# Kernel optimization log

Hardware: AMD Instinct MI355X
Metric: run time of the kernel (lower is better)

## Reference

```python
import jax, jax.numpy as jnp
import numpy as np
import math

N_A = 100000
N_B = 100000
E = 400000
D = 128      # in_dim == out_dim (skip connection requires equality)
H = 8        # n_heads
DK = 16      # d_k = D // H
SQRT_DK = math.sqrt(DK)


def setup_inputs():
    ks = list(jax.random.split(jax.random.key(0), 32))
    it = iter(ks)

    def nrm(shape, s):
        return (jax.random.normal(next(it), shape) * s).astype(jnp.float32)

    def idx(n):
        return jax.random.randint(next(it), (E,), 0, n)

    inp = {}
    inp['x_a'] = nrm((N_A, D), 1.0)
    inp['x_b'] = nrm((N_B, D), 1.0)
    inp['src_ab'], inp['dst_ab'] = idx(N_A), idx(N_B)
    inp['src_ba'], inp['dst_ba'] = idx(N_B), idx(N_A)
    inp['src_bb'], inp['dst_bb'] = idx(N_B), idx(N_B)
    w_scale = math.sqrt(2.0 / (D + D))  # xavier-ish
    for t in ('a', 'b'):
        for m in ('k', 'q', 'v', 'a'):
            inp['W%s_%s' % (m, t)] = nrm((D, D), w_scale)
            inp['b%s_%s' % (m, t)] = jnp.zeros((D,), jnp.float32)
        inp['skip_%s' % t] = jnp.ones((1,), jnp.float32)
    r_scale = math.sqrt(2.0 / (DK + DK))
    for e in ('ab', 'ba', 'bb'):
        inp['pri_%s' % e] = jnp.ones((H,), jnp.float32)
        inp['att_%s' % e] = nrm((H, DK, DK), r_scale)
        inp['msg_%s' % e] = nrm((H, DK, DK), r_scale)
    return inp


def _etype_agg(k_src, q_dst, v_src, src, dst, att_w, msg_w, pri, n_dst):
    # gather src/dst node features onto edges: [E, H, DK]
    ke = k_src[src]
    # bmm(k.transpose(1,0), relation_att).transpose(1,0) == einsum ehd,hdf->ehf
    key_e = jnp.einsum('ehd,hdf->ehf', ke, att_w)
    a = jnp.sum(q_dst[dst] * key_e, axis=-1) * pri / SQRT_DK   # [E, H]
    val = jnp.einsum('ehd,hdf->ehf', v_src[src], msg_w)         # [E, H, DK]
    # ragged per-dst-node softmax over incoming edges (DGL mailbox softmax)
    amax = jax.ops.segment_max(a, dst, num_segments=n_dst)
    amax = jax.lax.stop_gradient(jnp.where(jnp.isfinite(amax), amax, 0.0))
    ea = jnp.exp(a - amax[dst])
    denom = jax.ops.segment_sum(ea, dst, num_segments=n_dst)
    w = ea / jnp.maximum(denom[dst], 1e-9)
    h = jax.ops.segment_sum(w[:, :, None] * val, dst, num_segments=n_dst)
    return jax.nn.relu(h.reshape(n_dst, H * DK))


def reference(x_a, x_b, src_ab, dst_ab, src_ba, dst_ba, src_bb, dst_bb,
              Wk_a, bk_a, Wq_a, bq_a, Wv_a, bv_a, Wa_a, ba_a, skip_a,
              Wk_b, bk_b, Wq_b, bq_b, Wv_b, bv_b, Wa_b, ba_b, skip_b,
              pri_ab, att_ab, msg_ab, pri_ba, att_ba, msg_ba,
              pri_bb, att_bb, msg_bb):
    n_a, n_b = x_a.shape[0], x_b.shape[0]
    k_a = (x_a @ Wk_a + bk_a).reshape(n_a, H, DK)
    q_a = (x_a @ Wq_a + bq_a).reshape(n_a, H, DK)
    v_a = (x_a @ Wv_a + bv_a).reshape(n_a, H, DK)
    k_b = (x_b @ Wk_b + bk_b).reshape(n_b, H, DK)
    q_b = (x_b @ Wq_b + bq_b).reshape(n_b, H, DK)
    v_b = (x_b @ Wv_b + bv_b).reshape(n_b, H, DK)

    # per-etype attention + softmax + weighted aggregate
    t_b1 = _etype_agg(k_a, q_b, v_a, src_ab, dst_ab, att_ab, msg_ab, pri_ab, n_b)
    t_b2 = _etype_agg(k_b, q_b, v_b, src_bb, dst_bb, att_bb, msg_bb, pri_bb, n_b)
    t_b = 0.5 * (t_b1 + t_b2)        # cross_reducer='mean' over {ab, bb}
    t_a = _etype_agg(k_b, q_a, v_b, src_ba, dst_ba, att_ba, msg_ba, pri_ba, n_a)

    alpha_a = jax.nn.sigmoid(skip_a)
    out_a = (t_a @ Wa_a + ba_a) * alpha_a + x_a * (1.0 - alpha_a)
    alpha_b = jax.nn.sigmoid(skip_b)
    out_b = (t_b @ Wa_b + ba_b) * alpha_b + x_b * (1.0 - alpha_b)
    # dropout is identity in eval; use_norm=False
    return jnp.stack([out_a, out_b])  # [2, N, D]
```

## Files before the change

### kernel.cpp

```cpp
#include <hip/hip_runtime.h>
#include <hip/hip_bf16.h>
#include <stdint.h>

#define D 128
#define H 8
#define DK 16

#define SCAN_BLK 256
#define SCAN_ITEMS 8
#define SCAN_TILE (SCAN_BLK * SCAN_ITEMS)
#define NBUCK 192

typedef __attribute__((ext_vector_type(8))) short bf16x8;
typedef __attribute__((ext_vector_type(4))) float f32x4;

__device__ __forceinline__ unsigned short f2bf(float f) {
    unsigned int u = __float_as_uint(f);
    u = u + 0x7fffu + ((u >> 16) & 1u);
    return (unsigned short)(u >> 16);
}
__device__ __forceinline__ float bfl(unsigned int u) { return __uint_as_float(u << 16); }
__device__ __forceinline__ float bfh(unsigned int u) { return __uint_as_float(u & 0xffff0000u); }
__device__ __forceinline__ unsigned int pack2(unsigned short a, unsigned short b) {
    return (unsigned int)a | ((unsigned int)b << 16);
}
__device__ __forceinline__ void unpack8(uint4 u, float* o) {
    o[0]=bfl(u.x); o[1]=bfh(u.x); o[2]=bfl(u.y); o[3]=bfh(u.y);
    o[4]=bfl(u.z); o[5]=bfh(u.z); o[6]=bfl(u.w); o[7]=bfh(u.w);
}

struct WTIn  { const float* w[4]; };
struct WTOut { unsigned short* wt[4]; };
struct FoldArgs {
    const float* W[6]; const float* R[6]; const float* b[6];
    unsigned short* WT[6]; float* bf[6]; int mode[6];
};

__global__ __launch_bounds__(256) void prep_kernel(WTIn in, WTOut out, FoldArgs a,
                                                   int* __restrict__ cnt, int S,
                                                   int nz, int* __restrict__ dhd) {
    __shared__ float tile[32][33];
    __shared__ float Wl[128 * 17];
    __shared__ float Rl[256];
    int bid = blockIdx.x;
    int tid = threadIdx.x;
    if (bid < 64) {
        int mat = bid >> 4;
        int t = bid & 15;
        int k0 = (t >> 2) * 32, c0 = (t & 3) * 32;
        const float* W = in.w[mat];
        unsigned short* WT = out.wt[mat];
        int lr = tid >> 5, lc = tid & 31;
        #pragma unroll
        for (int p = 0; p < 4; ++p)
            tile[p * 8 + lr][lc] = W[(size_t)(k0 + p * 8 + lr) * D + c0 + lc];
        __syncthreads();
        #pragma unroll
        for (int p = 0; p < 4; ++p)
            WT[(size_t)(c0 + p * 8 + lr) * D + k0 + lc] = f2bf(tile[lc][p * 8 + lr]);
    } else if (bid < 112) {
        int v = (bid - 64) >> 3, h = (bid - 64) & 7;
        const float* W = a.W[v];
        #pragma unroll
        for (int p = 0; p < 8; ++p) {
            int idx = p * 256 + tid;
            int c = idx >> 4, i = idx & 15;
            Wl[c * 17 + i] = W[(size_t)c * D + h * 16 + i];
        }
        Rl[tid] = a.R[v][h * 256 + tid];
        __syncthreads();
        int mode = a.mode[v];
        int c = tid & 127, jb = (tid >> 7) * 8;
        #pragma unroll
        for (int jj = 0; jj < 8; ++jj) {
            int j = jb + jj;
            float s = 0.f;
            #pragma unroll
            for (int i = 0; i < 16; ++i)
                s = fmaf(Wl[c * 17 + i], mode ? Rl[i * 16 + j] : Rl[j * 16 + i], s);
            a.WT[v][(size_t)(h * 16 + j) * D + c] = f2bf(s);
        }
        if (tid < 16) {
            const float* b = a.b[v];
            float s = 0.f;
            #pragma unroll
            for (int i = 0; i < 16; ++i)
                s = fmaf(b[h * 16 + i], mode ? Rl[i * 16 + tid] : Rl[tid * 16 + i], s);
            a.bf[v][h * 16 + tid] = s;
        }
    } else if (bid < 112 + nz) {
        int base = (bid - 112) * 1024 + tid * 4;
        if (base + 4 <= S) {
            *(int4*)&cnt[base] = make_int4(0, 0, 0, 0);
        } else {
            for (int i = base; i < S; ++i) cnt[i] = 0;
        }
    } else {
        for (int i = tid; i < 2 * NBUCK; i += 256) dhd[i] = 0;
    }
}

#define ASTRIDE 136
struct ProjFusedArgs {
    const float* X[2];
    int N[2], nmat[2], nblk0;
    const unsigned short* wt[2][5];
    const float* bias[2][5];
    unsigned short* out[2][5];
};

__global__ __launch_bounds__(256) void proj_fused_kernel(ProjFusedArgs a)
{
    __shared__ unsigned short As[64 * ASTRIDE];
    __shared__ unsigned short Cs[64 * ASTRIDE];
    const int tid = threadIdx.x;
    const int w = tid >> 6;
    const int l = tid & 63;
    const int seg = (blockIdx.x >= a.nblk0) ? 1 : 0;
    const int row0 = (blockIdx.x - (seg ? a.nblk0 : 0)) * 64;
    const float* X = a.X[seg];
    const int N = a.N[seg];
    const int nm = a.nmat[seg];

    #pragma unroll
    for (int p = 0; p < 8; ++p) {
        int f = p * 256 + tid;
        int r = f >> 5;
        int c4 = f & 31;
        int row = row0 + r; if (row >= N) row = N - 1;
        float4 xv = *(const float4*)&X[(size_t)row * D + c4 * 4];
        unsigned int lo = pack2(f2bf(xv.x), f2bf(xv.y));
        unsigned int hi = pack2(f2bf(xv.z), f2bf(xv.w));
        *(uint2*)&As[r * ASTRIDE + c4 * 4] = make_uint2(lo, hi);
    }
    __syncthreads();

    const int lrow = l & 15;
    const int lk8 = (l >> 4) * 8;

    for (int m = 0; m < nm; ++m) {
        const unsigned short* WT = a.wt[seg][m];
        bf16x8 bfrag[2][4];
        #pragma unroll
        for (int cf = 0; cf < 2; ++cf)
            #pragma unroll
            for (int kc = 0; kc < 4; ++kc)
                bfrag[cf][kc] = *(const bf16x8*)&WT[(size_t)(w * 32 + cf * 16 + lrow) * D + kc * 32 + lk8];

        f32x4 acc[4][2];
        #pragma unroll
        for (int rf = 0; rf < 4; ++rf) {
            acc[rf][0] = (f32x4){0.f, 0.f, 0.f, 0.f};
            acc[rf][1] = (f32x4){0.f, 0.f, 0.f, 0.f};
        }
        #pragma unroll
        for (int rf = 0; rf < 4; ++rf) {
            bf16x8 afrag[4];
            #pragma unroll
            for (int kc = 0; kc < 4; ++kc)
                afrag[kc] = *(const bf16x8*)&As[(rf * 16 + lrow) * ASTRIDE + kc * 32 + lk8];
            #pragma unroll
            for (int kc = 0; kc < 4; ++kc) {
                acc[rf][0] = __builtin_amdgcn_mfma_f32_16x16x32_bf16(afrag[kc], bfrag[0][kc], acc[rf][0], 0, 0, 0);
                acc[rf][1] = __builtin_amdgcn_mfma_f32_16x16x32_bf16(afrag[kc], bfrag[1][kc], acc[rf][1], 0, 0, 0);
            }
        }
        float bias0 = a.bias[seg][m][w * 32 + lrow];
        float bias1 = a.bias[seg][m][w * 32 + 16 + lrow];
        #pragma unroll
        for (int rf = 0; rf < 4; ++rf) {
            #pragma unroll
            for (int r = 0; r < 4; ++r) {
                int lr = rf * 16 + (l >> 4) * 4 + r;
                Cs[lr * ASTRIDE + w * 32 + lrow]      = f2bf(acc[rf][0][r] + bias0);
                Cs[lr * ASTRIDE + w * 32 + 16 + lrow] = f2bf(acc[rf][1][r] + bias1);
            }
        }
        __syncthreads();
        unsigned short* O = a.out[seg][m];
        #pragma unroll
        for (int p = 0; p < 4; ++p) {
            int idx = p * 256 + tid;
            int r = idx >> 4, c8 = idx & 15;
            int row = row0 + r;
            if (row < N)
                *(uint4*)&O[(size_t)row * D + c8 * 8] = *(const uint4*)&Cs[r * ASTRIDE + c8 * 8];
        }
        __syncthreads();
    }
}

struct OutFusedArgs {
    const unsigned short* T1[2]; const unsigned short* T2[2];
    const unsigned short* WT[2]; const float* bias[2];
    const float* skip[2]; const float* X[2]; float* O[2];
    int N[2], nsrc[2], nblk0;
};

__global__ __launch_bounds__(256) void out_fused_kernel(OutFusedArgs a)
{
    __shared__ unsigned short As[64 * ASTRIDE];
    const int tid = threadIdx.x;
    const int w = tid >> 6;
    const int l = tid & 63;
    const int seg = (blockIdx.x >= a.nblk0) ? 1 : 0;
    const int row0 = (blockIdx.x - (seg ? a.nblk0 : 0)) * 64;
    const int N = a.N[seg];
    const int nsrc = a.nsrc[seg];
    const unsigned short* T1 = a.T1[seg];
    const unsigned short* T2 = a.T2[seg];

    #pragma unroll
    for (int p = 0; p < 4; ++p) {
        int idx = p * 256 + tid;
        int r = idx >> 4;
        int c8 = idx & 15;
        int row = row0 + r; if (row >= N) row = N - 1;
        uint4 tv = *(const uint4*)&T1[(size_t)row * D + c8 * 8];
        float v[8]; unpack8(tv, v);
        #pragma unroll
        for (int i = 0; i < 8; ++i) v[i] = fmaxf(v[i], 0.f);
        if (nsrc == 2) {
            uint4 uv = *(const uint4*)&T2[(size_t)row * D + c8 * 8];
            float u[8]; unpack8(uv, u);
            #pragma unroll
            for (int i = 0; i < 8; ++i) v[i] = 0.5f * (v[i] + fmaxf(u[i], 0.f));
        }
        uint4 pk;
        pk.x = pack2(f2bf(v[0]), f2bf(v[1]));
        pk.y = pack2(f2bf(v[2]), f2bf(v[3]));
        pk.z = pack2(f2bf(v[4]), f2bf(v[5]));
        pk.w = pack2(f2bf(v[6]), f2bf(v[7]));
        *(uint4*)&As[r * ASTRIDE + c8 * 8] = pk;
    }
    __syncthreads();

    const int lrow = l & 15;
    const int lk8 = (l >> 4) * 8;
    const unsigned short* WT = a.WT[seg];

    bf16x8 bfrag[2][4];
    #pragma unroll
    for (int cf = 0; cf < 2; ++cf)
        #pragma unroll
        for (int kc = 0; kc < 4; ++kc)
            bfrag[cf][kc] = *(const bf16x8*)&WT[(size_t)(w * 32 + cf * 16 + lrow) * D + kc * 32 + lk8];

    f32x4 acc[4][2];
    #pragma unroll
    for (int rf = 0; rf < 4; ++rf) {
        acc[rf][0] = (f32x4){0.f, 0.f, 0.f, 0.f};
        acc[rf][1] = (f32x4){0.f, 0.f, 0.f, 0.f};
    }
    #pragma unroll
    for (int rf = 0; rf < 4; ++rf) {
        bf16x8 afrag[4];
        #pragma unroll
        for (int kc = 0; kc < 4; ++kc)
            afrag[kc] = *(const bf16x8*)&As[(rf * 16 + lrow) * ASTRIDE + kc * 32 + lk8];
        #pragma unroll
        for (int kc = 0; kc < 4; ++kc) {
            acc[rf][0] = __builtin_amdgcn_mfma_f32_16x16x32_bf16(afrag[kc], bfrag[0][kc], acc[rf][0], 0, 0, 0);
            acc[rf][1] = __builtin_amdgcn_mfma_f32_16x16x32_bf16(afrag[kc], bfrag[1][kc], acc[rf][1], 0, 0, 0);
        }
    }
    float alpha = 1.f / (1.f + __expf(-a.skip[seg][0]));
    float om = 1.f - alpha;
    float bias0 = a.bias[seg][w * 32 + lrow];
    float bias1 = a.bias[seg][w * 32 + 16 + lrow];
    const float* X = a.X[seg];
    float* O = a.O[seg];
    #pragma unroll
    for (int rf = 0; rf < 4; ++rf) {
        #pragma unroll
        for (int r = 0; r < 4; ++r) {
            int row = row0 + rf * 16 + (l >> 4) * 4 + r;
            if (row < N) {
                int c0 = w * 32 + lrow;
                float x0 = X[(size_t)row * D + c0];
                float x1 = X[(size_t)row * D + c0 + 16];
                O[(size_t)row * D + c0]      = (acc[rf][0][r] + bias0) * alpha + x0 * om;
                O[(size_t)row * D + c0 + 16] = (acc[rf][1][r] + bias1) * alpha + x1 * om;
            }
        }
    }
}

struct EdgeArgs {
    const int* src[3]; const int* dst[3]; int base[3]; int E;
};

__global__ __launch_bounds__(256) void hist_all_kernel(EdgeArgs a, int* __restrict__ cnt) {
    int gid = blockIdx.x * 256 + threadIdx.x;
    int E = a.E;
    if (gid >= 3 * E) return;
    int t = (gid < E) ? 0 : ((gid < 2 * E) ? 1 : 2);
    int e = gid - t * E;
    atomicAdd(&cnt[a.base[t] + a.dst[t][e]], 1);
}

__global__ __launch_bounds__(SCAN_BLK) void scan1_kernel(
    const int* __restrict__ cnt, int* __restrict__ bsum,
    int* __restrict__ dhist, int n, int n_b)
{
    __shared__ int sh[SCAN_BLK];
    __shared__ int lh[NBUCK];
    int tid = threadIdx.x;
    if (tid < NBUCK) lh[tid] = 0;
    __syncthreads();
    int base = blockIdx.x * SCAN_TILE + tid * SCAN_ITEMS;
    int s = 0;
    #pragma unroll
    for (int i = 0; i < SCAN_ITEMS; ++i) {
        int idx = base + i;
        if (idx < n) {
            int d = cnt[idx];
            s += d;
            int t = (idx < n_b) ? 0 : ((idx < 2 * n_b) ? 1 : 2);
            int dc = d > 63 ? 63 : d;
            atomicAdd(&lh[t * 64 + 63 - dc], 1);
        }
    }
    sh[tid] = s; __syncthreads();
    for (int o = SCAN_BLK / 2; o > 0; o >>= 1) {
        if (tid < o) sh[tid] += sh[tid + o];
        __syncthreads();
    }
    if (tid == 0) bsum[blockIdx.x] = sh[0];
    if (tid < NBUCK && lh[tid]) atomicAdd(&dhist[tid], lh[tid]);
}

__global__ __launch_bounds__(SCAN_BLK) void scan3_kernel(
    const int* __restrict__ cnt, const int* __restrict__ bsum,
    int* __restrict__ offs, int* __restrict__ cursor, int n)
{
    __shared__ int red[SCAN_BLK];
    __shared__ int sh[SCAN_BLK];
    const int tid = threadIdx.x;
    int pre = 0;
    for (int i = tid; i < blockIdx.x; i += SCAN_BLK) pre += bsum[i];
    red[tid] = pre; __syncthreads();
    for (int o = SCAN_BLK / 2; o > 0; o >>= 1) {
        if (tid < o) red[tid] += red[tid + o];
        __syncthreads();
    }
    int base0 = red[0];

    int base = blockIdx.x * SCAN_TILE + tid * SCAN_ITEMS;
    int v[SCAN_ITEMS];
    int s = 0;
    #pragma unroll
    for (int i = 0; i < SCAN_ITEMS; ++i) {
        int idx = base + i;
        v[i] = (idx < n) ? cnt[idx] : 0;
        s += v[i];
    }
    sh[tid] = s; __syncthreads();
    for (int o = 1; o < SCAN_BLK; o <<= 1) {
        int t = (tid >= o) ? sh[tid - o] : 0;
        __syncthreads();
        sh[tid] += t;
        __syncthreads();
    }
    int off = base0 + sh[tid] - s;
    #pragma unroll
    for (int i = 0; i < SCAN_ITEMS; ++i) {
        int idx = base + i;
        if (idx < n) {
            offs[idx] = off;
            cursor[idx] = off;
            off += v[i];
            if (idx == n - 1) offs[n] = off;
        }
    }
}

__global__ __launch_bounds__(256) void scatter_all_kernel(
    EdgeArgs a, int* __restrict__ cursor, int* __restrict__ csr_src)
{
    int gid = blockIdx.x * 256 + threadIdx.x;
    int E = a.E;
    if (gid >= 3 * E) return;
    int t = (gid < E) ? 0 : ((gid < 2 * E) ? 1 : 2);
    int e = gid - t * E;
    int p = atomicAdd(&cursor[a.base[t] + a.dst[t][e]], 1);
    csr_src[p] = a.src[t][e];
}

__global__ __launch_bounds__(256) void deg_scatter_kernel(
    const int* __restrict__ cnt, const int* __restrict__ dhist, int* __restrict__ dcur,
    int* __restrict__ perm, int S, int n_b)
{
    __shared__ int sc[256];
    __shared__ int excl[NBUCK];
    __shared__ int lcnt[NBUCK];
    __shared__ int lbase[NBUCK];
    int tid = threadIdx.x;
    int v = (tid < NBUCK) ? dhist[tid] : 0;
    sc[tid] = v; __syncthreads();
    for (int o = 1; o < 256; o <<= 1) {
        int t = (tid >= o) ? sc[tid - o] : 0;
        __syncthreads();
        sc[tid] += t;
        __syncthreads();
    }
    if (tid < NBUCK) { excl[tid] = sc[tid] - v; lcnt[tid] = 0; }
    __syncthreads();
    int i = blockIdx.x * 256 + tid;
    bool valid = (i < S);
    int b = 0, r = 0;
    if (valid) {
        int t = (i < n_b) ? 0 : ((i < 2 * n_b) ? 1 : 2);
        int d = cnt[i]; if (d > 63) d = 63;
        b = t * 64 + 63 - d;
        r = atomicAdd(&lcnt[b], 1);
    }
    __syncthreads();
    if (tid < NBUCK && lcnt[tid]) lbase[tid] = excl[tid] + atomicAdd(&dcur[tid], lcnt[tid]);
    __syncthreads();
    if (valid) perm[lbase[b] + r] = i;
}

struct AggArgs {
    const unsigned short* K[3];
    const unsigned short* Q[3];
    const unsigned short* V[3];
    const float* pri[3];
    unsigned short* T[3];
};

__global__ __launch_bounds__(256) void csr_agg_all_kernel(
    const int* __restrict__ offs, const int* __restrict__ csr_src,
    const int* __restrict__ perm, AggArgs a, int n_b, int n_a)
{
    int gid = blockIdx.x * 256 + threadIdx.x;
    int si = gid >> 4;
    int hp = gid & 15;
    int h = hp >> 1, p = hp & 1;
    int S = 2 * n_b + n_a;
    if (si >= S) return;
    int s = perm[si];
    int t = (s < n_b) ? 0 : ((s < 2 * n_b) ? 1 : 2);
    int n = s - ((t == 2) ? 2 * n_b : t * n_b);

    const unsigned short *Kp, *Qp, *Vp; const float* prip; unsigned short* Tp;
    if (t == 0)      { Kp=a.K[0]; Qp=a.Q[0]; Vp=a.V[0]; prip=a.pri[0]; Tp=a.T[0]; }
    else if (t == 1) { Kp=a.K[1]; Qp=a.Q[1]; Vp=a.V[1]; prip=a.pri[1]; Tp=a.T[1]; }
    else             { Kp=a.K[2]; Qp=a.Q[2]; Vp=a.V[2]; prip=a.pri[2]; Tp=a.T[2]; }

    int e0 = offs[s], e1 = offs[s + 1];
    const int sub = h * DK + p * 8;

    uint4 q = *(const uint4*)(Qp + (size_t)n * D + sub);
    float qv[8]; unpack8(q, qv);
    float ps = prip[h] * 0.25f;

    float acc[8];
    #pragma unroll
    for (int i = 0; i < 8; ++i) acc[i] = 0.f;
    float den = 0.f;

    for (int e = e0; e < e1; ++e) {
        int sc = csr_src[e];
        uint4 k = *(const uint4*)(Kp + (size_t)sc * D + sub);
        uint4 v = *(const uint4*)(Vp + (size_t)sc * D + sub);
        float kv[8]; unpack8(k, kv);
        float d = 0.f;
        #pragma unroll
        for (int i = 0; i < 8; ++i) d = fmaf(kv[i], qv[i], d);
        d += __shfl_xor(d, 1, 64);
        float ea = __expf(d * ps);
        den += ea;
        float vv[8]; unpack8(v, vv);
        #pragma unroll
        for (int i = 0; i < 8; ++i) acc[i] = fmaf(ea, vv[i], acc[i]);
    }
    float inv = 1.f / fmaxf(den, 1e-9f);
    unsigned short ob[8];
    #pragma unroll
    for (int i = 0; i < 8; ++i) ob[i] = f2bf(acc[i] * inv);
    uint4 o0;
    o0.x = pack2(ob[0], ob[1]);  o0.y = pack2(ob[2], ob[3]);
    o0.z = pack2(ob[4], ob[5]);  o0.w = pack2(ob[6], ob[7]);
    *(uint4*)(Tp + (size_t)n * D + sub) = o0;
}

extern "C" void kernel_launch(void* const* d_in, const int* in_sizes, int n_in,
                              void* d_out, int out_size, void* d_ws, size_t ws_size,
                              hipStream_t stream) {
    const float* x_a = (const float*)d_in[0];
    const float* x_b = (const float*)d_in[1];
    const int* src_ab = (const int*)d_in[2];
    const int* dst_ab = (const int*)d_in[3];
    const int* src_ba = (const int*)d_in[4];
    const int* dst_ba = (const int*)d_in[5];
    const int* src_bb = (const int*)d_in[6];
    const int* dst_bb = (const int*)d_in[7];
    const float* Wk_a = (const float*)d_in[8];  const float* bk_a = (const float*)d_in[9];
    const float* Wq_a = (const float*)d_in[10]; const float* bq_a = (const float*)d_in[11];
    const float* Wv_a = (const float*)d_in[12]; const float* bv_a = (const float*)d_in[13];
    const float* Wa_a = (const float*)d_in[14]; const float* ba_a = (const float*)d_in[15];
    const float* skip_a = (const float*)d_in[16];
    const float* Wk_b = (const float*)d_in[17]; const float* bk_b = (const float*)d_in[18];
    const float* Wq_b = (const float*)d_in[19]; const float* bq_b = (const float*)d_in[20];
    const float* Wv_b = (const float*)d_in[21]; const float* bv_b = (const float*)d_in[22];
    const float* Wa_b = (const float*)d_in[23]; const float* ba_b = (const float*)d_in[24];
    const float* skip_b = (const float*)d_in[25];
    const float* pri_ab = (const float*)d_in[26];
    const float* att_ab = (const float*)d_in[27];
    const float* msg_ab = (const float*)d_in[28];
    const float* pri_ba = (const float*)d_in[29];
    const float* att_ba = (const float*)d_in[30];
    const float* msg_ba = (const float*)d_in[31];
    const float* pri_bb = (const float*)d_in[32];
    const float* att_bb = (const float*)d_in[33];
    const float* msg_bb = (const float*)d_in[34];

    const int n_a = in_sizes[0] / D;
    const int n_b = in_sizes[1] / D;
    const int E = in_sizes[2];
    const int S = 2 * n_b + n_a;

    size_t off = 0;
    char* base = (char*)d_ws;
    auto alloc = [&](size_t bytes) -> void* {
        void* r = base + off;
        off += (bytes + 255) & ~(size_t)255;
        return r;
    };
    unsigned short* k_a = (unsigned short*)alloc((size_t)n_a * D * 2);
    unsigned short* k_b = (unsigned short*)alloc((size_t)n_b * D * 2);
    unsigned short* qab = (unsigned short*)alloc((size_t)n_b * D * 2);
    unsigned short* qbb = (unsigned short*)alloc((size_t)n_b * D * 2);
    unsigned short* qba = (unsigned short*)alloc((size_t)n_a * D * 2);
    unsigned short* vab = (unsigned short*)alloc((size_t)n_a * D * 2);
    unsigned short* vbb = (unsigned short*)alloc((size_t)n_b * D * 2);
    unsigned short* vba = (unsigned short*)alloc((size_t)n_b * D * 2);
    unsigned short* t_a  = (unsigned short*)alloc((size_t)n_a * D * 2);
    unsigned short* t_b1 = (unsigned short*)alloc((size_t)n_b * D * 2);
    unsigned short* t_b2 = (unsigned short*)alloc((size_t)n_b * D * 2);
    int* cnt    = (int*)alloc((size_t)S * 4);
    int* offs   = (int*)alloc(((size_t)S + 1) * 4);
    int* cursor = (int*)alloc((size_t)S * 4);
    int* csr_src= (int*)alloc((size_t)3 * E * 4);
    int* bsum   = (int*)alloc(256 * 4);
    int* dhd    = (int*)alloc(2 * NBUCK * 4);
    int* dhist  = dhd;
    int* dcur   = dhd + NBUCK;
    int* perm   = (int*)alloc((size_t)S * 4);
    unsigned short* wt_plain[4];
    for (int i = 0; i < 4; ++i) wt_plain[i] = (unsigned short*)alloc((size_t)D * D * 2);
    unsigned short* wt_fold[6];
    float* bf_fold[6];
    for (int i = 0; i < 6; ++i) {
        wt_fold[i] = (unsigned short*)alloc((size_t)D * D * 2);
        bf_fold[i] = (float*)alloc((size_t)D * 4);
    }

    WTIn win; WTOut wout;
    const float* worig[4] = {Wk_a, Wk_b, Wa_a, Wa_b};
    for (int i = 0; i < 4; ++i) { win.w[i] = worig[i]; wout.wt[i] = wt_plain[i]; }
    FoldArgs fa;
    const float* fW[6] = {Wq_b, Wq_b, Wq_a, Wv_a, Wv_b, Wv_b};
    const float* fR[6] = {att_ab, att_bb, att_ba, msg_ab, msg_bb, msg_ba};
    const float* fb[6] = {bq_b, bq_b, bq_a, bv_a, bv_b, bv_b};
    int fm[6] = {0, 0, 0, 1, 1, 1};
    for (int i = 0; i < 6; ++i) {
        fa.W[i] = fW[i]; fa.R[i] = fR[i]; fa.b[i] = fb[i];
        fa.WT[i] = wt_fold[i]; fa.bf[i] = bf_fold[i]; fa.mode[i] = fm[i];
    }
    int nz = (S + 1023) / 1024;
    prep_kernel<<<112 + nz + 1, 256, 0, stream>>>(win, wout, fa, cnt, S, nz, dhd);

    EdgeArgs ea;
    ea.src[0] = src_ab; ea.dst[0] = dst_ab;
    ea.src[1] = src_bb; ea.dst[1] = dst_bb;
    ea.src[2] = src_ba; ea.dst[2] = dst_ba;
    ea.base[0] = 0; ea.base[1] = n_b; ea.base[2] = 2 * n_b;
    ea.E = E;
    int ge3 = (3 * E + 255) / 256;
    hist_all_kernel<<<ge3, 256, 0, stream>>>(ea, cnt);
    int nb = (S + SCAN_TILE - 1) / SCAN_TILE;
    scan1_kernel<<<nb, SCAN_BLK, 0, stream>>>(cnt, bsum, dhist, S, n_b);
    scan3_kernel<<<nb, SCAN_BLK, 0, stream>>>(cnt, bsum, offs, cursor, S);
    scatter_all_kernel<<<ge3, 256, 0, stream>>>(ea, cursor, csr_src);

    int gS = (S + 255) / 256;
    deg_scatter_kernel<<<gS, 256, 0, stream>>>(cnt, dhist, dcur, perm, S, n_b);

    const int gb_a = (n_a + 63) / 64;
    const int gb_b = (n_b + 63) / 64;
    ProjFusedArgs pa;
    pa.X[0] = x_a; pa.N[0] = n_a; pa.nmat[0] = 3;
    pa.X[1] = x_b; pa.N[1] = n_b; pa.nmat[1] = 5;
    pa.nblk0 = gb_a;
    pa.wt[0][0] = wt_plain[0]; pa.bias[0][0] = bk_a;       pa.out[0][0] = k_a;
    pa.wt[0][1] = wt_fold[2];  pa.bias[0][1] = bf_fold[2]; pa.out[0][1] = qba;
    pa.wt[0][2] = wt_fold[3];  pa.bias[0][2] = bf_fold[3]; pa.out[0][2] = vab;
    pa.wt[0][3] = wt_plain[0]; pa.bias[0][3] = bk_a;       pa.out[0][3] = k_a;
    pa.wt[0][4] = wt_plain[0]; pa.bias[0][4] = bk_a;       pa.out[0][4] = k_a;
    pa.wt[1][0] = wt_plain[1]; pa.bias[1][0] = bk_b;       pa.out[1][0] = k_b;
    pa.wt[1][1] = wt_fold[0];  pa.bias[1][1] = bf_fold[0]; pa.out[1][1] = qab;
    pa.wt[1][2] = wt_fold[1];  pa.bias[1][2] = bf_fold[1]; pa.out[1][2] = qbb;
    pa.wt[1][3] = wt_fold[4];  pa.bias[1][3] = bf_fold[4]; pa.out[1][3] = vbb;
    pa.wt[1][4] = wt_fold[5];  pa.bias[1][4] = bf_fold[5]; pa.out[1][4] = vba;
    proj_fused_kernel<<<gb_a + gb_b, 256, 0, stream>>>(pa);

    AggArgs aa;
    aa.K[0] = k_a; aa.Q[0] = qab; aa.V[0] = vab; aa.pri[0] = pri_ab; aa.T[0] = t_b1;
    aa.K[1] = k_b; aa.Q[1] = qbb; aa.V[1] = vbb; aa.pri[1] = pri_bb; aa.T[1] = t_b2;
    aa.K[2] = k_b; aa.Q[2] = qba; aa.V[2] = vba; aa.pri[2] = pri_ba; aa.T[2] = t_a;
    int gs = (S * 16 + 255) / 256;
    csr_agg_all_kernel<<<gs, 256, 0, stream>>>(offs, csr_src, perm, aa, n_b, n_a);

    float* out_a = (float*)d_out;
    float* out_b = (float*)d_out + (size_t)n_a * D;
    OutFusedArgs oa;
    oa.T1[0] = t_a;  oa.T2[0] = t_a;  oa.WT[0] = wt_plain[2]; oa.bias[0] = ba_a;
    oa.skip[0] = skip_a; oa.X[0] = x_a; oa.O[0] = out_a; oa.N[0] = n_a; oa.nsrc[0] = 1;
    oa.T1[1] = t_b1; oa.T2[1] = t_b2; oa.WT[1] = wt_plain[3]; oa.bias[1] = ba_b;
    oa.skip[1] = skip_b; oa.X[1] = x_b; oa.O[1] = out_b; oa.N[1] = n_b; oa.nsrc[1] = 2;
    oa.nblk0 = gb_a;
    out_fused_kernel<<<gb_a + gb_b, 256, 0, stream>>>(oa);
}
```

Baseline: 425.1 us.

## Overlap node projection GEMM with CSR build stages and unroll edge loop

Splits the projection GEMM into four chunks and co-schedules each chunk inside the histogram, scan1, scan3 and scatter/degree-sort launches, so independent work fills the otherwise underutilized small CSR-build kernels. This also removes the separate projection launch. Separately, the per-node aggregation loop is unrolled by two edges so the K and V gathers of two neighbors are in flight together. The merged kernels raise shared-memory footprint and register pressure for the light CSR blocks, which may reduce their occupancy.

```diff
diff --git a/kernel.cpp b/kernel.cpp
--- a/kernel.cpp
+++ b/kernel.cpp
@@ -101,23 +101,20 @@
 }
 
 #define ASTRIDE 136
-struct ProjFusedArgs {
+struct ProjChunk {
     const float* X[2];
-    int N[2], nmat[2], nblk0;
+    int N[2], nmat[2];
     const unsigned short* wt[2][5];
     const float* bias[2][5];
     unsigned short* out[2][5];
 };
 
-__global__ __launch_bounds__(256) void proj_fused_kernel(ProjFusedArgs a)
-{
+__device__ __forceinline__ void proj_body(const ProjChunk& a, int seg, int row0) {
     __shared__ unsigned short As[64 * ASTRIDE];
     __shared__ unsigned short Cs[64 * ASTRIDE];
     const int tid = threadIdx.x;
     const int w = tid >> 6;
     const int l = tid & 63;
-    const int seg = (blockIdx.x >= a.nblk0) ? 1 : 0;
-    const int row0 = (blockIdx.x - (seg ? a.nblk0 : 0)) * 64;
     const float* X = a.X[seg];
     const int N = a.N[seg];
     const int nm = a.nmat[seg];
@@ -190,108 +187,18 @@
     }
 }
 
-struct OutFusedArgs {
-    const unsigned short* T1[2]; const unsigned short* T2[2];
-    const unsigned short* WT[2]; const float* bias[2];
-    const float* skip[2]; const float* X[2]; float* O[2];
-    int N[2], nsrc[2], nblk0;
-};
-
-__global__ __launch_bounds__(256) void out_fused_kernel(OutFusedArgs a)
-{
-    __shared__ unsigned short As[64 * ASTRIDE];
-    const int tid = threadIdx.x;
-    const int w = tid >> 6;
-    const int l = tid & 63;
-    const int seg = (blockIdx.x >= a.nblk0) ? 1 : 0;
-    const int row0 = (blockIdx.x - (seg ? a.nblk0 : 0)) * 64;
-    const int N = a.N[seg];
-    const int nsrc = a.nsrc[seg];
-    const unsigned short* T1 = a.T1[seg];
-    const unsigned short* T2 = a.T2[seg];
-
-    #pragma unroll
-    for (int p = 0; p < 4; ++p) {
-        int idx = p * 256 + tid;
-        int r = idx >> 4;
-        int c8 = idx & 15;
-        int row = row0 + r; if (row >= N) row = N - 1;
-        uint4 tv = *(const uint4*)&T1[(size_t)row * D + c8 * 8];
-        float v[8]; unpack8(tv, v);
-        #pragma unroll
-        for (int i = 0; i < 8; ++i) v[i] = fmaxf(v[i], 0.f);
-        if (nsrc == 2) {
-            uint4 uv = *(const uint4*)&T2[(size_t)row * D + c8 * 8];
-            float u[8]; unpack8(uv, u);
-            #pragma unroll
-            for (int i = 0; i < 8; ++i) v[i] = 0.5f * (v[i] + fmaxf(u[i], 0.f));
-        }
-        uint4 pk;
-        pk.x = pack2(f2bf(v[0]), f2bf(v[1]));
-        pk.y = pack2(f2bf(v[2]), f2bf(v[3]));
-        pk.z = pack2(f2bf(v[4]), f2bf(v[5]));
-        pk.w = pack2(f2bf(v[6]), f2bf(v[7]));
-        *(uint4*)&As[r * ASTRIDE + c8 * 8] = pk;
-    }
-    __syncthreads();
-
-    const int lrow = l & 15;
-    const int lk8 = (l >> 4) * 8;
-    const unsigned short* WT = a.WT[seg];
-
-    bf16x8 bfrag[2][4];
-    #pragma unroll
-    for (int cf = 0; cf < 2; ++cf)
-        #pragma unroll
-        for (int kc = 0; kc < 4; ++kc)
-            bfrag[cf][kc] = *(const bf16x8*)&WT[(size_t)(w * 32 + cf * 16 + lrow) * D + kc * 32 + lk8];
-
-    f32x4 acc[4][2];
-    #pragma unroll
-    for (int rf = 0; rf < 4; ++rf) {
-        acc[rf][0] = (f32x4){0.f, 0.f, 0.f, 0.f};
-        acc[rf][1] = (f32x4){0.f, 0.f, 0.f, 0.f};
-    }
-    #pragma unroll
-    for (int rf = 0; rf < 4; ++rf) {
-        bf16x8 afrag[4];
-        #pragma unroll
-        for (int kc = 0; kc < 4; ++kc)
-            afrag[kc] = *(const bf16x8*)&As[(rf * 16 + lrow) * ASTRIDE + kc * 32 + lk8];
-        #pragma unroll
-        for (int kc = 0; kc < 4; ++kc) {
-            acc[rf][0] = __builtin_amdgcn_mfma_f32_16x16x32_bf16(afrag[kc], bfrag[0][kc], acc[rf][0], 0, 0, 0);
-            acc[rf][1] = __builtin_amdgcn_mfma_f32_16x16x32_bf16(afrag[kc], bfrag[1][kc], acc[rf][1], 0, 0, 0);
-        }
-    }
-    float alpha = 1.f / (1.f + __expf(-a.skip[seg][0]));
-    float om = 1.f - alpha;
-    float bias0 = a.bias[seg][w * 32 + lrow];
-    float bias1 = a.bias[seg][w * 32 + 16 + lrow];
-    const float* X = a.X[seg];
-    float* O = a.O[seg];
-    #pragma unroll
-    for (int rf = 0; rf < 4; ++rf) {
-        #pragma unroll
-        for (int r = 0; r < 4; ++r) {
-            int row = row0 + rf * 16 + (l >> 4) * 4 + r;
-            if (row < N) {
-                int c0 = w * 32 + lrow;
-                float x0 = X[(size_t)row * D + c0];
-                float x1 = X[(size_t)row * D + c0 + 16];
-                O[(size_t)row * D + c0]      = (acc[rf][0][r] + bias0) * alpha + x0 * om;
-                O[(size_t)row * D + c0 + 16] = (acc[rf][1][r] + bias1) * alpha + x1 * om;
-            }
-        }
-    }
+__device__ __forceinline__ void proj_dispatch(const ProjChunk& pc, int local,
+                                              int blkA, int rowA0, int rowB0) {
+    if (local < blkA) proj_body(pc, 0, rowA0 + local * 64);
+    else              proj_body(pc, 1, rowB0 + (local - blkA) * 64);
 }
 
 struct EdgeArgs {
     const int* src[3]; const int* dst[3]; int base[3]; int E;
 };
 
-__global__ __launch_bounds__(256) void hist_all_kernel(EdgeArgs a, int* __restrict__ cnt) {
-    int gid = blockIdx.x * 256 + threadIdx.x;
+__device__ __forceinline__ void hist_body(const EdgeArgs& a, int* cnt, int bid) {
+    int gid = bid * 256 + threadIdx.x;
     int E = a.E;
     if (gid >= 3 * E) return;
     int t = (gid < E) ? 0 : ((gid < 2 * E) ? 1 : 2);
@@ -299,16 +206,14 @@
     atomicAdd(&cnt[a.base[t] + a.dst[t][e]], 1);
 }
 
-__global__ __launch_bounds__(SCAN_BLK) void scan1_kernel(
-    const int* __restrict__ cnt, int* __restrict__ bsum,
-    int* __restrict__ dhist, int n, int n_b)
-{
+__device__ __forceinline__ void scan1_body(const int* cnt, int* bsum, int* dhist,
+                                           int n, int n_b, int bid) {
     __shared__ int sh[SCAN_BLK];
     __shared__ int lh[NBUCK];
     int tid = threadIdx.x;
     if (tid < NBUCK) lh[tid] = 0;
     __syncthreads();
-    int base = blockIdx.x * SCAN_TILE + tid * SCAN_ITEMS;
+    int base = bid * SCAN_TILE + tid * SCAN_ITEMS;
     int s = 0;
     #pragma unroll
     for (int i = 0; i < SCAN_ITEMS; ++i) {
@@ -326,19 +231,17 @@
         if (tid < o) sh[tid] += sh[tid + o];
         __syncthreads();
     }
-    if (tid == 0) bsum[blockIdx.x] = sh[0];
+    if (tid == 0) bsum[bid] = sh[0];
     if (tid < NBUCK && lh[tid]) atomicAdd(&dhist[tid], lh[tid]);
 }
 
-__global__ __launch_bounds__(SCAN_BLK) void scan3_kernel(
-    const int* __restrict__ cnt, const int* __restrict__ bsum,
-    int* __restrict__ offs, int* __restrict__ cursor, int n)
-{
+__device__ __forceinline__ void scan3_body(const int* cnt, const int* bsum,
+                                           int* offs, int* cursor, int n, int bid) {
     __shared__ int red[SCAN_BLK];
     __shared__ int sh[SCAN_BLK];
     const int tid = threadIdx.x;
     int pre = 0;
-    for (int i = tid; i < blockIdx.x; i += SCAN_BLK) pre += bsum[i];
+    for (int i = tid; i < bid; i += SCAN_BLK) pre += bsum[i];
     red[tid] = pre; __syncthreads();
     for (int o = SCAN_BLK / 2; o > 0; o >>= 1) {
         if (tid < o) red[tid] += red[tid + o];
@@ -346,7 +249,7 @@
     }
     int base0 = red[0];
 
-    int base = blockIdx.x * SCAN_TILE + tid * SCAN_ITEMS;
+    int base = bid * SCAN_TILE + tid * SCAN_ITEMS;
     int v[SCAN_ITEMS];
     int s = 0;
     #pragma unroll
@@ -375,10 +278,9 @@
     }
 }
 
-__global__ __launch_bounds__(256) void scatter_all_kernel(
-    EdgeArgs a, int* __restrict__ cursor, int* __restrict__ csr_src)
-{
-    int gid = blockIdx.x * 256 + threadIdx.x;
+__device__ __forceinline__ void scatter_body(const EdgeArgs& a, int* cursor,
+                                             int* csr_src, int bid) {
+    int gid = bid * 256 + threadIdx.x;
     int E = a.E;
     if (gid >= 3 * E) return;
     int t = (gid < E) ? 0 : ((gid < 2 * E) ? 1 : 2);
@@ -387,10 +289,8 @@
     csr_src[p] = a.src[t][e];
 }
 
-__global__ __launch_bounds__(256) void deg_scatter_kernel(
-    const int* __restrict__ cnt, const int* __restrict__ dhist, int* __restrict__ dcur,
-    int* __restrict__ perm, int S, int n_b)
-{
+__device__ __forceinline__ void deg_scatter_body(const int* cnt, const int* dhist,
+                                                 int* dcur, int* perm, int S, int n_b, int bid) {
     __shared__ int sc[256];
     __shared__ int excl[NBUCK];
     __shared__ int lcnt[NBUCK];
@@ -406,7 +306,7 @@
     }
     if (tid < NBUCK) { excl[tid] = sc[tid] - v; lcnt[tid] = 0; }
     __syncthreads();
-    int i = blockIdx.x * 256 + tid;
+    int i = bid * 256 + tid;
     bool valid = (i < S);
     int b = 0, r = 0;
     if (valid) {
@@ -419,6 +319,40 @@
     if (tid < NBUCK && lcnt[tid]) lbase[tid] = excl[tid] + atomicAdd(&dcur[tid], lcnt[tid]);
     __syncthreads();
     if (valid) perm[lbase[b] + r] = i;
+}
+
+__global__ __launch_bounds__(256) void stageA_kernel(EdgeArgs ea, int* __restrict__ cnt,
+    ProjChunk pc, int csrBlk, int blkA, int rowA0, int rowB0)
+{
+    if ((int)blockIdx.x < csrBlk) hist_body(ea, cnt, blockIdx.x);
+    else proj_dispatch(pc, blockIdx.x - csrBlk, blkA, rowA0, rowB0);
+}
+
+__global__ __launch_bounds__(256) void stageB_kernel(const int* __restrict__ cnt,
+    int* __restrict__ bsum, int* __restrict__ dhist, int S, int n_b,
+    ProjChunk pc, int csrBlk, int blkA, int rowA0, int rowB0)
+{
+    if ((int)blockIdx.x < csrBlk) scan1_body(cnt, bsum, dhist, S, n_b, blockIdx.x);
+    else proj_dispatch(pc, blockIdx.x - csrBlk, blkA, rowA0, rowB0);
+}
+
+__global__ __launch_bounds__(256) void stageC_kernel(const int* __restrict__ cnt,
+    const int* __restrict__ bsum, int* __restrict__ offs, int* __restrict__ cursor, int S,
+    ProjChunk pc, int csrBlk, int blkA, int rowA0, int rowB0)
+{
+    if ((int)blockIdx.x < csrBlk) scan3_body(cnt, bsum, offs, cursor, S, blockIdx.x);
+    else proj_dispatch(pc, blockIdx.x - csrBlk, blkA, rowA0, rowB0);
+}
+
+__global__ __launch_bounds__(256) void stageD_kernel(EdgeArgs ea, int* __restrict__ cursor,
+    int* __restrict__ csr_src, const int* __restrict__ cnt, const int* __restrict__ dhist,
+    int* __restrict__ dcur, int* __restrict__ perm, int S, int n_b,
+    ProjChunk pc, int csrBlk, int degBlk, int blkA, int rowA0, int rowB0)
+{
+    int bid = blockIdx.x;
+    if (bid < csrBlk) scatter_body(ea, cursor, csr_src, bid);
+    else if (bid < csrBlk + degBlk) deg_scatter_body(cnt, dhist, dcur, perm, S, n_b, bid - csrBlk);
+    else proj_dispatch(pc, bid - csrBlk - degBlk, blkA, rowA0, rowB0);
 }
 
 struct AggArgs {
@@ -460,10 +394,36 @@
     for (int i = 0; i < 8; ++i) acc[i] = 0.f;
     float den = 0.f;
 
-    for (int e = e0; e < e1; ++e) {
-        int sc = csr_src[e];
-        uint4 k = *(const uint4*)(Kp + (size_t)sc * D + sub);
-        uint4 v = *(const uint4*)(Vp + (size_t)sc * D + sub);
+    int e = e0;
+    for (; e + 2 <= e1; e += 2) {
+        int s0 = csr_src[e], s1 = csr_src[e + 1];
+        uint4 k0 = *(const uint4*)(Kp + (size_t)s0 * D + sub);
+        uint4 v0 = *(const uint4*)(Vp + (size_t)s0 * D + sub);
+        uint4 k1 = *(const uint4*)(Kp + (size_t)s1 * D + sub);
+        uint4 v1 = *(const uint4*)(Vp + (size_t)s1 * D + sub);
+        float ka[8], kb[8];
+        unpack8(k0, ka); unpack8(k1, kb);
+        float d0 = 0.f, d1 = 0.f;
+        #pragma unroll
+        for (int i = 0; i < 8; ++i) {
+            d0 = fmaf(ka[i], qv[i], d0);
+            d1 = fmaf(kb[i], qv[i], d1);
+        }
+        d0 += __shfl_xor(d0, 1, 64);
+        d1 += __shfl_xor(d1, 1, 64);
+        float ea0 = __expf(d0 * ps);
+        float ea1 = __expf(d1 * ps);
+        den += ea0 + ea1;
+        float va[8], vb[8];
+        unpack8(v0, va); unpack8(v1, vb);
+        #pragma unroll
+        for (int i = 0; i < 8; ++i)
+            acc[i] = fmaf(ea0, va[i], fmaf(ea1, vb[i], acc[i]));
+    }
+    if (e < e1) {
+        int s0 = csr_src[e];
+        uint4 k = *(const uint4*)(Kp + (size_t)s0 * D + sub);
+        uint4 v = *(const uint4*)(Vp + (size_t)s0 * D + sub);
         float kv[8]; unpack8(k, kv);
         float d = 0.f;
         #pragma unroll
@@ -483,6 +443,102 @@
     o0.x = pack2(ob[0], ob[1]);  o0.y = pack2(ob[2], ob[3]);
     o0.z = pack2(ob[4], ob[5]);  o0.w = pack2(ob[6], ob[7]);
     *(uint4*)(Tp + (size_t)n * D + sub) = o0;
+}
+
+struct OutFusedArgs {
+    const unsigned short* T1[2]; const unsigned short* T2[2];
+    const unsigned short* WT[2]; const float* bias[2];
+    const float* skip[2]; const float* X[2]; float* O[2];
+    int N[2], nsrc[2], nblk0;
+};
+
+__global__ __launch_bounds__(256) void out_fused_kernel(OutFusedArgs a)
+{
+    __shared__ unsigned short As[64 * ASTRIDE];
+    const int tid = threadIdx.x;
+    const int w = tid >> 6;
+    const int l = tid & 63;
+    const int seg = (blockIdx.x >= a.nblk0) ? 1 : 0;
+    const int row0 = (blockIdx.x - (seg ? a.nblk0 : 0)) * 64;
+    const int N = a.N[seg];
+    const int nsrc = a.nsrc[seg];
+    const unsigned short* T1 = a.T1[seg];
+    const unsigned short* T2 = a.T2[seg];
+
+    #pragma unroll
+    for (int p = 0; p < 4; ++p) {
+        int idx = p * 256 + tid;
+        int r = idx >> 4;
+        int c8 = idx & 15;
+        int row = row0 + r; if (row >= N) row = N - 1;
+        uint4 tv = *(const uint4*)&T1[(size_t)row * D + c8 * 8];
+        float v[8]; unpack8(tv, v);
+        #pragma unroll
+        for (int i = 0; i < 8; ++i) v[i] = fmaxf(v[i], 0.f);
+        if (nsrc == 2) {
+            uint4 uv = *(const uint4*)&T2[(size_t)row * D + c8 * 8];
+            float u[8]; unpack8(uv, u);
+            #pragma unroll
+            for (int i = 0; i < 8; ++i) v[i] = 0.5f * (v[i] + fmaxf(u[i], 0.f));
+        }
+        uint4 pk;
+        pk.x = pack2(f2bf(v[0]), f2bf(v[1]));
+        pk.y = pack2(f2bf(v[2]), f2bf(v[3]));
+        pk.z = pack2(f2bf(v[4]), f2bf(v[5]));
+        pk.w = pack2(f2bf(v[6]), f2bf(v[7]));
+        *(uint4*)&As[r * ASTRIDE + c8 * 8] = pk;
+    }
+    __syncthreads();
+
+    const int lrow = l & 15;
+    const int lk8 = (l >> 4) * 8;
+    const unsigned short* WT = a.WT[seg];
+
+    bf16x8 bfrag[2][4];
+    #pragma unroll
+    for (int cf = 0; cf < 2; ++cf)
+        #pragma unroll
+        for (int kc = 0; kc < 4; ++kc)
+            bfrag[cf][kc] = *(const bf16x8*)&WT[(size_t)(w * 32 + cf * 16 + lrow) * D + kc * 32 + lk8];
+
+    f32x4 acc[4][2];
+    #pragma unroll
+    for (int rf = 0; rf < 4; ++rf) {
+        acc[rf][0] = (f32x4){0.f, 0.f, 0.f, 0.f};
+        acc[rf][1] = (f32x4){0.f, 0.f, 0.f, 0.f};
+    }
+    #pragma unroll
+    for (int rf = 0; rf < 4; ++rf) {
+        bf16x8 afrag[4];
+        #pragma unroll
+        for (int kc = 0; kc < 4; ++kc)
+            afrag[kc] = *(const bf16x8*)&As[(rf * 16 + lrow) * ASTRIDE + kc * 32 + lk8];
+        #pragma unroll
+        for (int kc = 0; kc < 4; ++kc) {
+            acc[rf][0] = __builtin_amdgcn_mfma_f32_16x16x32_bf16(afrag[kc], bfrag[0][kc], acc[rf][0], 0, 0, 0);
+            acc[rf][1] = __builtin_amdgcn_mfma_f32_16x16x32_bf16(afrag[kc], bfrag[1][kc], acc[rf][1], 0, 0, 0);
+        }
+    }
+    float alpha = 1.f / (1.f + __expf(-a.skip[seg][0]));
+    float om = 1.f - alpha;
+    float bias0 = a.bias[seg][w * 32 + lrow];
+    float bias1 = a.bias[seg][w * 32 + 16 + lrow];
+    const float* X = a.X[seg];
+    float* O = a.O[seg];
+    #pragma unroll
+    for (int rf = 0; rf < 4; ++rf) {
+        #pragma unroll
+        for (int r = 0; r < 4; ++r) {
+            int row = row0 + rf * 16 + (l >> 4) * 4 + r;
+            if (row < N) {
+                int c0 = w * 32 + lrow;
+                float x0 = X[(size_t)row * D + c0];
+                float x1 = X[(size_t)row * D + c0 + 16];
+                O[(size_t)row * D + c0]      = (acc[rf][0][r] + bias0) * alpha + x0 * om;
+                O[(size_t)row * D + c0 + 16] = (acc[rf][1][r] + bias1) * alpha + x1 * om;
+            }
+        }
+    }
 }
 
 extern "C" void kernel_launch(void* const* d_in, const int* in_sizes, int n_in,
@@ -579,32 +635,47 @@
     ea.base[0] = 0; ea.base[1] = n_b; ea.base[2] = 2 * n_b;
     ea.E = E;
     int ge3 = (3 * E + 255) / 256;
-    hist_all_kernel<<<ge3, 256, 0, stream>>>(ea, cnt);
     int nb = (S + SCAN_TILE - 1) / SCAN_TILE;
-    scan1_kernel<<<nb, SCAN_BLK, 0, stream>>>(cnt, bsum, dhist, S, n_b);
-    scan3_kernel<<<nb, SCAN_BLK, 0, stream>>>(cnt, bsum, offs, cursor, S);
-    scatter_all_kernel<<<ge3, 256, 0, stream>>>(ea, cursor, csr_src);
-
     int gS = (S + 255) / 256;
-    deg_scatter_kernel<<<gS, 256, 0, stream>>>(cnt, dhist, dcur, perm, S, n_b);
+
+    ProjChunk pc;
+    pc.X[0] = x_a; pc.N[0] = n_a; pc.nmat[0] = 3;
+    pc.X[1] = x_b; pc.N[1] = n_b; pc.nmat[1] = 5;
+    pc.wt[0][0] = wt_plain[0]; pc.bias[0][0] = bk_a;       pc.out[0][0] = k_a;
+    pc.wt[0][1] = wt_fold[2];  pc.bias[0][1] = bf_fold[2]; pc.out[0][1] = qba;
+    pc.wt[0][2] = wt_fold[3];  pc.bias[0][2] = bf_fold[3]; pc.out[0][2] = vab;
+    pc.wt[0][3] = wt_plain[0]; pc.bias[0][3] = bk_a;       pc.out[0][3] = k_a;
+    pc.wt[0][4] = wt_plain[0]; pc.bias[0][4] = bk_a;       pc.out[0][4] = k_a;
+    pc.wt[1][0] = wt_plain[1]; pc.bias[1][0] = bk_b;       pc.out[1][0] = k_b;
+    pc.wt[1][1] = wt_fold[0];  pc.bias[1][1] = bf_fold[0]; pc.out[1][1] = qab;
+    pc.wt[1][2] = wt_fold[1];  pc.bias[1][2] = bf_fold[1]; pc.out[1][2] = qbb;
+    pc.wt[1][3] = wt_fold[4];  pc.bias[1][3] = bf_fold[4]; pc.out[1][3] = vbb;
+    pc.wt[1][4] = wt_fold[5];  pc.bias[1][4] = bf_fold[5]; pc.out[1][4] = vba;
 
     const int gb_a = (n_a + 63) / 64;
     const int gb_b = (n_b + 63) / 64;
-    ProjFusedArgs pa;
-    pa.X[0] = x_a; pa.N[0] = n_a; pa.nmat[0] = 3;
-    pa.X[1] = x_b; pa.N[1] = n_b; pa.nmat[1] = 5;
-    pa.nblk0 = gb_a;
-    pa.wt[0][0] = wt_plain[0]; pa.bias[0][0] = bk_a;       pa.out[0][0] = k_a;
-    pa.wt[0][1] = wt_fold[2];  pa.bias[0][1] = bf_fold[2]; pa.out[0][1] = qba;
-    pa.wt[0][2] = wt_fold[3];  pa.bias[0][2] = bf_fold[3]; pa.out[0][2] = vab;
-    pa.wt[0][3] = wt_plain[0]; pa.bias[0][3] = bk_a;       pa.out[0][3] = k_a;
-    pa.wt[0][4] = wt_plain[0]; pa.bias[0][4] = bk_a;       pa.out[0][4] = k_a;
-    pa.wt[1][0] = wt_plain[1]; pa.bias[1][0] = bk_b;       pa.out[1][0] = k_b;
-    pa.wt[1][1] = wt_fold[0];  pa.bias[1][1] = bf_fold[0]; pa.out[1][1] = qab;
-    pa.wt[1][2] = wt_fold[1];  pa.bias[1][2] = bf_fold[1]; pa.out[1][2] = qbb;
-    pa.wt[1][3] = wt_fold[4];  pa.bias[1][3] = bf_fold[4]; pa.out[1][3] = vbb;
-    pa.wt[1][4] = wt_fold[5];  pa.bias[1][4] = bf_fold[5]; pa.out[1][4] = vba;
-    proj_fused_kernel<<<gb_a + gb_b, 256, 0, stream>>>(pa);
+    const int splitA = (gb_a + 3) / 4;
+    const int splitB = (gb_b + 3) / 4;
+    auto chunkA = [&](int s) { int r = gb_a - s * splitA; return r < 0 ? 0 : (r > splitA ? splitA : r); };
+    auto chunkB = [&](int s) { int r = gb_b - s * splitB; return r < 0 ? 0 : (r > splitB ? splitB : r); };
+
+    {
+        int bA = chunkA(0), bB = chunkB(0);
+        stageA_kernel<<<ge3 + bA + bB, 256, 0, stream>>>(ea, cnt, pc, ge3, bA, 0, 0);
+    }
+    {
+        int bA = chunkA(1), bB = chunkB(1);
+        stageB_kernel<<<nb + bA + bB, 256, 0, stream>>>(cnt, bsum, dhist, S, n_b, pc, nb, bA, splitA * 64, splitB * 64);
+    }
+    {
+        int bA = chunkA(2), bB = chunkB(2);
+        stageC_kernel<<<nb + bA + bB, 256, 0, stream>>>(cnt, bsum, offs, cursor, S, pc, nb, bA, 2 * splitA * 64, 2 * splitB * 64);
+    }
+    {
+        int bA = chunkA(3), bB = chunkB(3);
+        stageD_kernel<<<ge3 + gS + bA + bB, 256, 0, stream>>>(ea, cursor, csr_src, cnt, dhist, dcur, perm, S, n_b,
+                                                              pc, ge3, gS, bA, 3 * splitA * 64, 3 * splitB * 64);
+    }
 
     AggArgs aa;
     aa.K[0] = k_a; aa.Q[0] = qab; aa.V[0] = vab; aa.pri[0] = pri_ab; aa.T[0] = t_b1;
```

New measurement: 432.0 us. Within noise of the previous version (+1.6%).
